# Performance work log

Measured on AMD Instinct MI355X. Metric: run time of the kernel, lower is better.

Reference implementation:

```python
import jax, jax.numpy as jnp
import numpy as np

N_HEADS = 8


def setup_inputs() -> dict:
    key = jax.random.key(0)
    qkv = jax.random.normal(key, (4, 1536, 2048), dtype=jnp.float32)
    return {"qkv": qkv}


def reference(qkv) -> jnp.ndarray:
    bs, width, length = qkv.shape
    assert width % (3 * N_HEADS) == 0
    ch = width // (3 * N_HEADS)
    # [bs*H, 3*ch, T] -> split into q, k, v each [bs*H, ch, T]
    qkv_ = qkv.reshape(bs * N_HEADS, 3 * ch, length)
    q, k, v = qkv_[:, :ch], qkv_[:, ch:2 * ch], qkv_[:, 2 * ch:]
    scale = 1.0 / np.sqrt(np.sqrt(ch)).astype(np.float32)
    # scores [bs*H, T_q, T_k]
    weight = jnp.einsum('bct,bcs->bts', q * scale, k * scale)
    # NOTE: faithful to source — softmax over dim=1 (the query axis t), in float32
    weight = jax.nn.softmax(weight.astype(jnp.float32), axis=1).astype(weight.dtype)
    a = jnp.einsum('bts,bcs->bct', weight, v)  # [bs*H, ch, T]
    return a.reshape(bs, N_HEADS * ch, length)
```

## Files before the change

kernel.cpp:

```cpp
#include <hip/hip_runtime.h>
#include <hip/hip_bf16.h>


#define SEQ   2048
#define CHD   64
#define NHB   32
#define SCALE_QK 0.42466090f

typedef short bf16x8 __attribute__((ext_vector_type(8)));
typedef float f32x4  __attribute__((ext_vector_type(4)));
typedef float f32x16 __attribute__((ext_vector_type(16)));
typedef unsigned int   u32x4 __attribute__((ext_vector_type(4)));
typedef unsigned short us8   __attribute__((ext_vector_type(8)));

extern "C" __device__ float __ocml_native_exp2_f32(float);
#define EXP2(x) __ocml_native_exp2_f32(x)

__device__ __forceinline__ unsigned short f2bf(float f) {
    unsigned int u = __builtin_bit_cast(unsigned int, f);
    u += 0x7FFFu + ((u >> 16) & 1u);
    return (unsigned short)(u >> 16);
}

__device__ __forceinline__ void gl_lds16(const void* g, void* l) {
    __builtin_amdgcn_global_load_lds(
        (const __attribute__((address_space(1))) void*)g,
        (__attribute__((address_space(3))) void*)l, 16, 0, 0);
}

__device__ __forceinline__ unsigned cvtpk(float a, float b) {
    unsigned r;
    asm("v_cvt_pk_bf16_f32 %0, %1, %2" : "=v"(r) : "v"(a), "v"(b));
    return r;
}
__device__ __forceinline__ void plswap(unsigned &a, unsigned &b) {
    asm("v_permlane32_swap_b32 %0, %1" : "+v"(a), "+v"(b));
}

#define ZERO16 {0.f,0.f,0.f,0.f,0.f,0.f,0.f,0.f,0.f,0.f,0.f,0.f,0.f,0.f,0.f,0.f}

__global__ __launch_bounds__(256) void convert_qk(
    const float* __restrict__ qkv, unsigned short* __restrict__ Qt,
    unsigned short* __restrict__ Kt)
{
    __shared__ float Tl[64][129];
    const int bid = blockIdx.x;
    const int head = bid >> 4, t0 = (bid & 15) * 128;
    const int b = head >> 3, h = head & 7;
    const float* base = qkv + (size_t)(b * 1536 + h * 192) * SEQ;
    const int tid = threadIdx.x;
#pragma unroll
    for (int pp = 0; pp < 2; ++pp) {
        const float* src = base + (size_t)(pp ? CHD : 0) * SEQ;
        unsigned short* dst = (pp ? Kt : Qt) + (size_t)head * SEQ * CHD;
        if (pp) __syncthreads();
        for (int e = tid; e < 8192; e += 256) {
            int c = e >> 7, ti = e & 127;
            Tl[c][ti] = src[(size_t)c * SEQ + t0 + ti];
        }
        __syncthreads();
        for (int g = tid; g < 1024; g += 256) {
            int t = g >> 3, cg = g & 7;
            us8 u;
#pragma unroll
            for (int j = 0; j < 8; ++j) u[j] = f2bf(Tl[cg * 8 + j][t] * SCALE_QK);
            *(us8*)(dst + (size_t)(t0 + t) * 64 + ((cg * 8) ^ ((t & 7) << 3))) = u;
        }
    }
}

__global__ __launch_bounds__(512, 2) void stats10_kernel(
    const float* __restrict__ qkv, const unsigned short* __restrict__ Qt,
    const unsigned short* __restrict__ Kt, unsigned short* __restrict__ Vb)
{
    __shared__ __attribute__((aligned(16))) unsigned short Qs[4][4096];
    __shared__ float rlb[256];
    const int bid = blockIdx.x;
    const int bs  = ((bid & 7) << 5) | (bid >> 3);
    const int head = bs >> 3, s0 = (bs & 7) * 256;
    const int b = head >> 3, h = head & 7;
    const char* Qhb = (const char*)(Qt + (size_t)head * SEQ * CHD);
    const unsigned short* Kh = Kt + (size_t)head * SEQ * CHD;
    const int tid = threadIdx.x, w = tid >> 6, l = tid & 63, lo5 = l & 31, hi = l >> 5;
    const int rsw = (lo5 & 7) << 3;

    bf16x8 kfr[4];
#pragma unroll
    for (int kc = 0; kc < 4; ++kc)
        kfr[kc] = *(const bf16x8*)(
            Kh + (size_t)(s0 + w * 32 + lo5) * 64 + (((kc << 4) + (hi << 3)) ^ rsw));

    auto stage = [&](int p, int tc) {
        gl_lds16(Qhb + (size_t)tc * 8192 + tid * 16, &Qs[p][0] + tid * 8);
    };

    float lacc[4] = {0.f, 0.f, 0.f, 0.f};

    stage(0, 0);
    stage(1, 1);
    for (int tc = 0; tc < 32; ++tc) {
        if (tc < 31) asm volatile("s_waitcnt vmcnt(1)" ::: "memory");
        else         asm volatile("s_waitcnt vmcnt(0)" ::: "memory");
        __builtin_amdgcn_s_barrier();
        __builtin_amdgcn_sched_barrier(0);
        if (tc < 30) stage((tc + 2) & 3, tc + 2);
        const unsigned short* qs = &Qs[tc & 3][0];
        __builtin_amdgcn_s_setprio(1);
#pragma unroll
        for (int ts = 0; ts < 2; ++ts) {
            f32x16 s = ZERO16;
#pragma unroll
            for (int kc = 0; kc < 4; ++kc) {
                bf16x8 qa = *(const bf16x8*)(
                    qs + (ts * 32 + lo5) * 64 + (((kc << 4) + (hi << 3)) ^ rsw));
                s = __builtin_amdgcn_mfma_f32_32x32x16_bf16(qa, kfr[kc], s, 0, 0, 0);
            }
#pragma unroll
            for (int r = 0; r < 16; ++r) lacc[r & 3] += EXP2(s[r]);
        }
        __builtin_amdgcn_s_setprio(0);
    }

    float lsum = (lacc[0] + lacc[1]) + (lacc[2] + lacc[3]);
    lsum += __shfl_xor(lsum, 32);
    if (l < 32) rlb[w * 32 + lo5] = 1.0f / lsum;
    __syncthreads();

    const float* vp = qkv + (size_t)(b * 1536 + h * 192 + 2 * CHD) * SEQ;
    unsigned short* Vh = Vb + (size_t)head * SEQ * CHD;
    for (int g = tid; g < 2048; g += 512) {
        int c = g >> 5, si8 = (g & 31) * 8;
        const float* vrow = vp + (size_t)c * SEQ + s0 + si8;
        f32x4 v0 = *(const f32x4*)(vrow);
        f32x4 v1 = *(const f32x4*)(vrow + 4);
        us8 u;
#pragma unroll
        for (int j = 0; j < 4; ++j) u[j]     = f2bf(v0[j] * rlb[si8 + j]);
#pragma unroll
        for (int j = 0; j < 4; ++j) u[4 + j] = f2bf(v1[j] * rlb[si8 + 4 + j]);
        int swb = (si8 & ~63) | ((si8 & 63) ^ ((c & 7) << 3));
        *(us8*)(Vh + (size_t)c * SEQ + s0 + swb) = u;
    }
}

__global__ __launch_bounds__(512, 1) void attn13_kernel(
    const unsigned short* __restrict__ Qt, const unsigned short* __restrict__ Kt,
    const unsigned short* __restrict__ Vb, float* __restrict__ out)
{
    __shared__ __attribute__((aligned(16))) unsigned short KV[4][8192];
    const int bid = blockIdx.x;
    const int bs  = ((bid & 7) << 5) | (bid >> 3);
    const int head = bs >> 3, t0 = (bs & 7) * 256;
    const int b = head >> 3, h = head & 7;
    const int tid = threadIdx.x, w = tid >> 6, l = tid & 63, lo5 = l & 31, hi = l >> 5;
    const int tw = w >> 1, sh = w & 1;
    const int rsw = (lo5 & 7) << 3;
    const unsigned short* Qh = Qt + (size_t)head * SEQ * CHD;
    const char* Khb = (const char*)(Kt + (size_t)head * SEQ * CHD);
    const char* Vhb = (const char*)(Vb + (size_t)head * SEQ * CHD);

    bf16x8 qfA[4], qfB[4];
#pragma unroll
    for (int kc = 0; kc < 4; ++kc) {
        qfA[kc] = *(const bf16x8*)(
            Qh + (size_t)(t0 + tw * 64 + lo5) * 64 + (((kc << 4) + (hi << 3)) ^ rsw));
        qfB[kc] = *(const bf16x8*)(
            Qh + (size_t)(t0 + tw * 64 + 32 + lo5) * 64 + (((kc << 4) + (hi << 3)) ^ rsw));
    }

    f32x16 accA0 = ZERO16, accA1 = ZERO16, accB0 = ZERO16, accB1 = ZERO16;

    const int vc = tid >> 3, vs16 = (tid & 7) * 16;
    auto stage = [&](int p, int cj) {
        unsigned short* kb = &KV[p][0];
        unsigned short* vb = &KV[p][4096];
        gl_lds16(Khb + (size_t)cj * 8192 + tid * 16, kb + tid * 8);
        gl_lds16(Vhb + (size_t)vc * 4096 + (size_t)cj * 128 + vs16, vb + tid * 8);
    };

    stage(0, 0);
    stage(1, 1);

    for (int j = 0; j < 32; ++j) {
        const int p = j & 3;
        if (j < 31) asm volatile("s_waitcnt vmcnt(2)" ::: "memory");
        else        asm volatile("s_waitcnt vmcnt(0)" ::: "memory");
        __builtin_amdgcn_s_barrier();
        __builtin_amdgcn_sched_barrier(0);
        if (j < 30) stage((j + 2) & 3, j + 2);

        const unsigned short* kb = &KV[p][0];
        const unsigned short* vb = &KV[p][4096];

        bf16x8 kf[4], vf0k0, vf0k1, vf1k0, vf1k1;
#pragma unroll
        for (int kc = 0; kc < 4; ++kc)
            kf[kc] = *(const bf16x8*)(
                kb + (sh * 32 + lo5) * 64 + (((kc << 4) + (hi << 3)) ^ rsw));
        vf0k0 = *(const bf16x8*)(vb + (lo5) * 64       + ((sh * 32 +      (hi << 3)) ^ rsw));
        vf0k1 = *(const bf16x8*)(vb + (lo5) * 64       + ((sh * 32 + 16 + (hi << 3)) ^ rsw));
        vf1k0 = *(const bf16x8*)(vb + (32 + lo5) * 64  + ((sh * 32 +      (hi << 3)) ^ rsw));
        vf1k1 = *(const bf16x8*)(vb + (32 + lo5) * 64  + ((sh * 32 + 16 + (hi << 3)) ^ rsw));

        __builtin_amdgcn_s_setprio(1);
        f32x16 SA = ZERO16, SB = ZERO16;
#pragma unroll
        for (int kc = 0; kc < 4; ++kc)
            SA = __builtin_amdgcn_mfma_f32_32x32x16_bf16(kf[kc], qfA[kc], SA, 0, 0, 0);
#pragma unroll
        for (int kc = 0; kc < 4; ++kc)
            SB = __builtin_amdgcn_mfma_f32_32x32x16_bf16(kf[kc], qfB[kc], SB, 0, 0, 0);

        {
            float p16[16];
#pragma unroll
            for (int r = 0; r < 16; ++r) p16[r] = EXP2(SA[r]);
            unsigned w0 = cvtpk(p16[0],  p16[1]),  w1 = cvtpk(p16[2],  p16[3]);
            unsigned w2 = cvtpk(p16[4],  p16[5]),  w3 = cvtpk(p16[6],  p16[7]);
            unsigned w4 = cvtpk(p16[8],  p16[9]),  w5 = cvtpk(p16[10], p16[11]);
            unsigned w6 = cvtpk(p16[12], p16[13]), w7 = cvtpk(p16[14], p16[15]);
            plswap(w0, w2); plswap(w1, w3); plswap(w4, w6); plswap(w5, w7);
            bf16x8 pfA = __builtin_bit_cast(bf16x8, (u32x4){w0, w1, w2, w3});
            bf16x8 pfB = __builtin_bit_cast(bf16x8, (u32x4){w4, w5, w6, w7});
            accA0 = __builtin_amdgcn_mfma_f32_32x32x16_bf16(vf0k0, pfA, accA0, 0, 0, 0);
            accA0 = __builtin_amdgcn_mfma_f32_32x32x16_bf16(vf0k1, pfB, accA0, 0, 0, 0);
            accA1 = __builtin_amdgcn_mfma_f32_32x32x16_bf16(vf1k0, pfA, accA1, 0, 0, 0);
            accA1 = __builtin_amdgcn_mfma_f32_32x32x16_bf16(vf1k1, pfB, accA1, 0, 0, 0);
        }
        {
            float p16[16];
#pragma unroll
            for (int r = 0; r < 16; ++r) p16[r] = EXP2(SB[r]);
            unsigned w0 = cvtpk(p16[0],  p16[1]),  w1 = cvtpk(p16[2],  p16[3]);
            unsigned w2 = cvtpk(p16[4],  p16[5]),  w3 = cvtpk(p16[6],  p16[7]);
            unsigned w4 = cvtpk(p16[8],  p16[9]),  w5 = cvtpk(p16[10], p16[11]);
            unsigned w6 = cvtpk(p16[12], p16[13]), w7 = cvtpk(p16[14], p16[15]);
            plswap(w0, w2); plswap(w1, w3); plswap(w4, w6); plswap(w5, w7);
            bf16x8 pfA = __builtin_bit_cast(bf16x8, (u32x4){w0, w1, w2, w3});
            bf16x8 pfB = __builtin_bit_cast(bf16x8, (u32x4){w4, w5, w6, w7});
            accB0 = __builtin_amdgcn_mfma_f32_32x32x16_bf16(vf0k0, pfA, accB0, 0, 0, 0);
            accB0 = __builtin_amdgcn_mfma_f32_32x32x16_bf16(vf0k1, pfB, accB0, 0, 0, 0);
            accB1 = __builtin_amdgcn_mfma_f32_32x32x16_bf16(vf1k0, pfA, accB1, 0, 0, 0);
            accB1 = __builtin_amdgcn_mfma_f32_32x32x16_bf16(vf1k1, pfB, accB1, 0, 0, 0);
        }
        __builtin_amdgcn_s_setprio(0);
    }

    __syncthreads();
    float* red = (float*)&KV[0][0];
    if (sh == 0) {
        *(f32x16*)(red + (size_t)w * 2048 + l * 16)        = accA1;
        *(f32x16*)(red + (size_t)w * 2048 + 1024 + l * 16) = accB1;
    } else {
        *(f32x16*)(red + (size_t)w * 2048 + l * 16)        = accA0;
        *(f32x16*)(red + (size_t)w * 2048 + 1024 + l * 16) = accB0;
    }
    __syncthreads();
    f32x16 pA = *(const f32x16*)(red + (size_t)(w ^ 1) * 2048 + l * 16);
    f32x16 pB = *(const f32x16*)(red + (size_t)(w ^ 1) * 2048 + 1024 + l * 16);
    f32x16 finA, finB;
    if (sh == 0) { finA = accA0 + pA; finB = accB0 + pB; }
    else         { finA = accA1 + pA; finB = accB1 + pB; }

    float* op = out + (size_t)(b * 512 + h * 64) * SEQ;
    const int tA = t0 + tw * 64 + lo5, tB = tA + 32;
#pragma unroll
    for (int r = 0; r < 16; ++r) {
        int c = sh * 32 + (r & 3) + 8 * (r >> 2) + 4 * hi;
        op[(size_t)c * SEQ + tA] = finA[r];
        op[(size_t)c * SEQ + tB] = finB[r];
    }
}


__device__ __forceinline__ bf16x8 lds_frag(const unsigned short* base, int row, int el) {
    int e = el ^ ((row & 7) << 3);
    return *(const bf16x8*)(base + row * 64 + e);
}

__global__ __launch_bounds__(256) void qkv_stats_kernel(
    const float* __restrict__ qkv, float* __restrict__ m_ws, float* __restrict__ rl_ws)
{
    __shared__ __attribute__((aligned(16))) unsigned short Kl[128 * 64];
    __shared__ __attribute__((aligned(16))) unsigned short Ql[64 * 64];
    const int head = blockIdx.x >> 4, stile = blockIdx.x & 15, s0 = stile * 128;
    const int b = head >> 3, h = head & 7;
    const float* qp = qkv + (size_t)(b * 1536 + h * 192) * SEQ;
    const float* kp = qp + (size_t)CHD * SEQ;
    const int tid = threadIdx.x, w = tid >> 6, l = tid & 63, lg = l >> 4, lr = l & 15;
    for (int idx = tid; idx < 128 * 64; idx += 256) {
        int s = idx & 127, c = idx >> 7;
        Kl[s * 64 + (c ^ ((s & 7) << 3))] = f2bf(kp[(size_t)c * SEQ + s0 + s]);
    }
    float m_run[2] = {-__builtin_inff(), -__builtin_inff()};
    float l_run[2] = {0.f, 0.f};
    for (int chunk = 0; chunk < 32; ++chunk) {
        const int t0 = chunk * 64;
        __syncthreads();
        for (int idx = tid; idx < 64 * 64; idx += 256) {
            int t = idx & 63, c = idx >> 6;
            Ql[t * 64 + (c ^ ((t & 7) << 3))] = f2bf(qp[(size_t)c * SEQ + t0 + t]);
        }
        __syncthreads();
#pragma unroll
        for (int ntl = 0; ntl < 2; ++ntl) {
            const int srow = 16 * (2 * w + ntl) + lr;
            float vals[16];
#pragma unroll
            for (int mt = 0; mt < 4; ++mt) {
                f32x4 sacc = {0.f, 0.f, 0.f, 0.f};
#pragma unroll
                for (int kk = 0; kk < 2; ++kk) {
                    bf16x8 a  = lds_frag(Ql, 16 * mt + lr, 32 * kk + 8 * lg);
                    bf16x8 bk = lds_frag(Kl, srow,         32 * kk + 8 * lg);
                    sacc = __builtin_amdgcn_mfma_f32_16x16x32_bf16(a, bk, sacc, 0, 0, 0);
                }
#pragma unroll
                for (int j = 0; j < 4; ++j) vals[mt * 4 + j] = sacc[j] * 0.125f;
            }
            float cm = vals[0];
#pragma unroll
            for (int i = 1; i < 16; ++i) cm = fmaxf(cm, vals[i]);
            cm = fmaxf(cm, __shfl_xor(cm, 16));
            cm = fmaxf(cm, __shfl_xor(cm, 32));
            float newm = fmaxf(m_run[ntl], cm);
            l_run[ntl] *= __expf(m_run[ntl] - newm);
            m_run[ntl] = newm;
            float ps = 0.f;
#pragma unroll
            for (int i = 0; i < 16; ++i) ps += __expf(vals[i] - newm);
            ps += __shfl_xor(ps, 16);
            ps += __shfl_xor(ps, 32);
            l_run[ntl] += ps;
        }
    }
    if (lg == 0) {
#pragma unroll
        for (int ntl = 0; ntl < 2; ++ntl) {
            int sg = s0 + 16 * (2 * w + ntl) + lr;
            m_ws[head * SEQ + sg]  = m_run[ntl];
            rl_ws[head * SEQ + sg] = 1.0f / l_run[ntl];
        }
    }
}

__global__ __launch_bounds__(256) void qkv_attn_kernel(
    const float* __restrict__ qkv, const float* __restrict__ m_ws,
    const float* __restrict__ rl_ws, float* __restrict__ out)
{
    __shared__ __attribute__((aligned(16))) unsigned short Ql[128 * 64];
    __shared__ __attribute__((aligned(16))) unsigned short Kl[64 * 64];
    __shared__ __attribute__((aligned(16))) unsigned short Vl[64 * 64];
    __shared__ __attribute__((aligned(16))) unsigned short Pl[128 * 64];
    const int head = blockIdx.x >> 4, ttile = blockIdx.x & 15, t0 = ttile * 128;
    const int b = head >> 3, h = head & 7;
    const float* qp  = qkv + (size_t)(b * 1536 + h * 192) * SEQ;
    const float* kp  = qp + (size_t)CHD * SEQ;
    const float* vp  = qp + (size_t)(2 * CHD) * SEQ;
    const float* mh  = m_ws  + head * SEQ;
    const float* rlh = rl_ws + head * SEQ;
    const int tid = threadIdx.x, w = tid >> 6, l = tid & 63, lg = l >> 4, lr = l & 15;
    for (int idx = tid; idx < 128 * 64; idx += 256) {
        int t = idx & 127, c = idx >> 7;
        Ql[t * 64 + (c ^ ((t & 7) << 3))] = f2bf(qp[(size_t)c * SEQ + t0 + t]);
    }
    f32x4 acc[4][2];
#pragma unroll
    for (int i = 0; i < 4; ++i)
#pragma unroll
        for (int j = 0; j < 2; ++j) acc[i][j] = (f32x4){0.f, 0.f, 0.f, 0.f};
    for (int sc = 0; sc < 32; ++sc) {
        const int s0 = sc * 64;
        __syncthreads();
        for (int idx = tid; idx < 64 * 64; idx += 256) {
            int s = idx & 63, c = idx >> 6;
            Kl[s * 64 + (c ^ ((s & 7) << 3))] = f2bf(kp[(size_t)c * SEQ + s0 + s]);
            Vl[c * 64 + (s ^ ((c & 7) << 3))] = f2bf(vp[(size_t)c * SEQ + s0 + s] * rlh[s0 + s]);
        }
        __syncthreads();
        float msv[4];
#pragma unroll
        for (int nts = 0; nts < 4; ++nts) msv[nts] = mh[s0 + 16 * nts + lr];
#pragma unroll
        for (int mts = 0; mts < 2; ++mts) {
            const int trowbase = 16 * (2 * w + mts);
#pragma unroll
            for (int nts = 0; nts < 4; ++nts) {
                f32x4 sa = {0.f, 0.f, 0.f, 0.f};
#pragma unroll
                for (int kk = 0; kk < 2; ++kk) {
                    bf16x8 a  = lds_frag(Ql, trowbase + lr, 32 * kk + 8 * lg);
                    bf16x8 bk = lds_frag(Kl, 16 * nts + lr, 32 * kk + 8 * lg);
                    sa = __builtin_amdgcn_mfma_f32_16x16x32_bf16(a, bk, sa, 0, 0, 0);
                }
                const int scol = 16 * nts + lr;
#pragma unroll
                for (int j = 0; j < 4; ++j) {
                    int trow = trowbase + 4 * lg + j;
                    float p = __expf(sa[j] * 0.125f - msv[nts]);
                    Pl[trow * 64 + (scol ^ ((trow & 7) << 3))] = f2bf(p);
                }
            }
        }
#pragma unroll
        for (int mt = 0; mt < 4; ++mt) {
#pragma unroll
            for (int ntl = 0; ntl < 2; ++ntl) {
                const int trow = 16 * (2 * w + ntl);
#pragma unroll
                for (int kk = 0; kk < 2; ++kk) {
                    bf16x8 a  = lds_frag(Vl, 16 * mt + lr, 32 * kk + 8 * lg);
                    bf16x8 bp = lds_frag(Pl, trow + lr,    32 * kk + 8 * lg);
                    acc[mt][ntl] = __builtin_amdgcn_mfma_f32_16x16x32_bf16(a, bp, acc[mt][ntl], 0, 0, 0);
                }
            }
        }
    }
    float* op = out + (size_t)(b * 512 + h * 64) * SEQ;
#pragma unroll
    for (int mt = 0; mt < 4; ++mt) {
#pragma unroll
        for (int ntl = 0; ntl < 2; ++ntl) {
            int tcol = t0 + 16 * (2 * w + ntl) + lr;
#pragma unroll
            for (int j = 0; j < 4; ++j) {
                int c = 16 * mt + 4 * lg + j;
                op[(size_t)c * SEQ + tcol] = acc[mt][ntl][j];
            }
        }
    }
}

extern "C" void kernel_launch(void* const* d_in, const int* in_sizes, int n_in,
                              void* d_out, int out_size, void* d_ws, size_t ws_size,
                              hipStream_t stream) {
    const float* qkv = (const float*)d_in[0];
    float* out = (float*)d_out;
    (void)in_sizes; (void)n_in; (void)out_size;

    const size_t need = (size_t)3 * NHB * SEQ * CHD * 2;
    if (ws_size >= need) {
        unsigned short* Qt = (unsigned short*)d_ws;
        unsigned short* Kt = Qt + (size_t)NHB * SEQ * CHD;
        unsigned short* Vb = Kt + (size_t)NHB * SEQ * CHD;
        convert_qk    <<<dim3(NHB * 16), dim3(256), 0, stream>>>(qkv, Qt, Kt);
        stats10_kernel<<<dim3(256),      dim3(512), 0, stream>>>(qkv, Qt, Kt, Vb);
        attn13_kernel <<<dim3(256),      dim3(512), 0, stream>>>(Qt, Kt, Vb, out);
    } else {
        float* m_ws  = (float*)d_ws;
        float* rl_ws = m_ws + (size_t)NHB * SEQ;
        qkv_stats_kernel<<<dim3(NHB * 16), dim3(256), 0, stream>>>(qkv, m_ws, rl_ws);
        qkv_attn_kernel <<<dim3(NHB * 16), dim3(256), 0, stream>>>(qkv, m_ws, rl_ws, out);
    }
}
```

Before: 82.80 us.

## Split stats and attention kernels along reduction axis with atomic accumulation

The column-sum stats kernel is split in two. One kernel computes partial sums over half the query range and combines them with atomic adds. A second kernel scales V by the reciprocal sums. The attention kernel likewise splits the key dimension in half across twice as many blocks and accumulates output with atomic adds after memsetting it. This doubles grid size to fill more CUs on a 256-CU part, at the cost of extra memsets, an additional launch, and atomic traffic on the output.

```diff
diff --git a/kernel.cpp b/kernel.cpp
--- a/kernel.cpp
+++ b/kernel.cpp
@@ -69,66 +69,78 @@
     }
 }
 
-__global__ __launch_bounds__(512, 2) void stats10_kernel(
-    const float* __restrict__ qkv, const unsigned short* __restrict__ Qt,
-    const unsigned short* __restrict__ Kt, unsigned short* __restrict__ Vb)
+__global__ __launch_bounds__(512, 4) void statsA_kernel(
+    const unsigned short* __restrict__ Qt, const unsigned short* __restrict__ Kt,
+    float* __restrict__ l_ws)
 {
     __shared__ __attribute__((aligned(16))) unsigned short Qs[4][4096];
+    const int bid = blockIdx.x;
+    const int bs  = ((bid & 7) << 6) | (bid >> 3);
+    const int head = bs >> 4, s0 = ((bs >> 1) & 7) * 256, tH = bs & 1;
+    const char* Qhb = (const char*)(Qt + (size_t)head * SEQ * CHD);
+    const unsigned short* Kh = Kt + (size_t)head * SEQ * CHD;
+    const int tid = threadIdx.x, w = tid >> 6, l = tid & 63, lo5 = l & 31, hi = l >> 5;
+    const int rsw = (lo5 & 7) << 3;
+
+    bf16x8 kfr[4];
+#pragma unroll
+    for (int kc = 0; kc < 4; ++kc)
+        kfr[kc] = *(const bf16x8*)(
+            Kh + (size_t)(s0 + w * 32 + lo5) * 64 + (((kc << 4) + (hi << 3)) ^ rsw));
+
+    auto stage = [&](int p, int tc) {
+        gl_lds16(Qhb + (size_t)(tH * 16 + tc) * 8192 + tid * 16, &Qs[p][0] + tid * 8);
+    };
+
+    float lacc[4] = {0.f, 0.f, 0.f, 0.f};
+
+    stage(0, 0);
+    stage(1, 1);
+    for (int tc = 0; tc < 16; ++tc) {
+        if (tc < 15) asm volatile("s_waitcnt vmcnt(1)" ::: "memory");
+        else         asm volatile("s_waitcnt vmcnt(0)" ::: "memory");
+        __builtin_amdgcn_s_barrier();
+        __builtin_amdgcn_sched_barrier(0);
+        if (tc < 14) stage((tc + 2) & 3, tc + 2);
+        const unsigned short* qs = &Qs[tc & 3][0];
+        __builtin_amdgcn_s_setprio(1);
+#pragma unroll
+        for (int ts = 0; ts < 2; ++ts) {
+            f32x16 s = ZERO16;
+#pragma unroll
+            for (int kc = 0; kc < 4; ++kc) {
+                bf16x8 qa = *(const bf16x8*)(
+                    qs + (ts * 32 + lo5) * 64 + (((kc << 4) + (hi << 3)) ^ rsw));
+                s = __builtin_amdgcn_mfma_f32_32x32x16_bf16(qa, kfr[kc], s, 0, 0, 0);
+            }
+#pragma unroll
+            for (int r = 0; r < 16; ++r) lacc[r & 3] += EXP2(s[r]);
+        }
+        __builtin_amdgcn_s_setprio(0);
+    }
+
+    float lsum = (lacc[0] + lacc[1]) + (lacc[2] + lacc[3]);
+    lsum += __shfl_xor(lsum, 32);
+    if (l < 32) unsafeAtomicAdd(&l_ws[head * SEQ + s0 + w * 32 + lo5], lsum);
+}
+
+__global__ __launch_bounds__(256) void statsB_kernel(
+    const float* __restrict__ qkv, const float* __restrict__ l_ws,
+    unsigned short* __restrict__ Vb)
+{
     __shared__ float rlb[256];
     const int bid = blockIdx.x;
     const int bs  = ((bid & 7) << 5) | (bid >> 3);
     const int head = bs >> 3, s0 = (bs & 7) * 256;
     const int b = head >> 3, h = head & 7;
-    const char* Qhb = (const char*)(Qt + (size_t)head * SEQ * CHD);
-    const unsigned short* Kh = Kt + (size_t)head * SEQ * CHD;
-    const int tid = threadIdx.x, w = tid >> 6, l = tid & 63, lo5 = l & 31, hi = l >> 5;
-    const int rsw = (lo5 & 7) << 3;
-
-    bf16x8 kfr[4];
-#pragma unroll
-    for (int kc = 0; kc < 4; ++kc)
-        kfr[kc] = *(const bf16x8*)(
-            Kh + (size_t)(s0 + w * 32 + lo5) * 64 + (((kc << 4) + (hi << 3)) ^ rsw));
-
-    auto stage = [&](int p, int tc) {
-        gl_lds16(Qhb + (size_t)tc * 8192 + tid * 16, &Qs[p][0] + tid * 8);
-    };
-
-    float lacc[4] = {0.f, 0.f, 0.f, 0.f};
-
-    stage(0, 0);
-    stage(1, 1);
-    for (int tc = 0; tc < 32; ++tc) {
-        if (tc < 31) asm volatile("s_waitcnt vmcnt(1)" ::: "memory");
-        else         asm volatile("s_waitcnt vmcnt(0)" ::: "memory");
-        __builtin_amdgcn_s_barrier();
-        __builtin_amdgcn_sched_barrier(0);
-        if (tc < 30) stage((tc + 2) & 3, tc + 2);
-        const unsigned short* qs = &Qs[tc & 3][0];
-        __builtin_amdgcn_s_setprio(1);
-#pragma unroll
-        for (int ts = 0; ts < 2; ++ts) {
-            f32x16 s = ZERO16;
-#pragma unroll
-            for (int kc = 0; kc < 4; ++kc) {
-                bf16x8 qa = *(const bf16x8*)(
-                    qs + (ts * 32 + lo5) * 64 + (((kc << 4) + (hi << 3)) ^ rsw));
-                s = __builtin_amdgcn_mfma_f32_32x32x16_bf16(qa, kfr[kc], s, 0, 0, 0);
-            }
-#pragma unroll
-            for (int r = 0; r < 16; ++r) lacc[r & 3] += EXP2(s[r]);
-        }
-        __builtin_amdgcn_s_setprio(0);
-    }
-
-    float lsum = (lacc[0] + lacc[1]) + (lacc[2] + lacc[3]);
-    lsum += __shfl_xor(lsum, 32);
-    if (l < 32) rlb[w * 32 + lo5] = 1.0f / lsum;
+    const int tid = threadIdx.x;
+
+    rlb[tid] = 1.0f / l_ws[head * SEQ + s0 + tid];
     __syncthreads();
 
     const float* vp = qkv + (size_t)(b * 1536 + h * 192 + 2 * CHD) * SEQ;
     unsigned short* Vh = Vb + (size_t)head * SEQ * CHD;
-    for (int g = tid; g < 2048; g += 512) {
+    for (int g = tid; g < 2048; g += 256) {
         int c = g >> 5, si8 = (g & 31) * 8;
         const float* vrow = vp + (size_t)c * SEQ + s0 + si8;
         f32x4 v0 = *(const f32x4*)(vrow);
@@ -143,14 +155,15 @@
     }
 }
 
-__global__ __launch_bounds__(512, 1) void attn13_kernel(
+__global__ __launch_bounds__(512, 4) void attnA_kernel(
     const unsigned short* __restrict__ Qt, const unsigned short* __restrict__ Kt,
     const unsigned short* __restrict__ Vb, float* __restrict__ out)
 {
     __shared__ __attribute__((aligned(16))) unsigned short KV[4][8192];
     const int bid = blockIdx.x;
-    const int bs  = ((bid & 7) << 5) | (bid >> 3);
-    const int head = bs >> 3, t0 = (bs & 7) * 256;
+    const int bs  = ((bid & 7) << 6) | (bid >> 3);
+    const int head = bs >> 4, t0 = ((bs >> 1) & 7) * 256, sH = bs & 1;
+    const int cbase = sH * 16;
     const int b = head >> 3, h = head & 7;
     const int tid = threadIdx.x, w = tid >> 6, l = tid & 63, lo5 = l & 31, hi = l >> 5;
     const int tw = w >> 1, sh = w & 1;
@@ -178,16 +191,16 @@
         gl_lds16(Vhb + (size_t)vc * 4096 + (size_t)cj * 128 + vs16, vb + tid * 8);
     };
 
-    stage(0, 0);
-    stage(1, 1);
-
-    for (int j = 0; j < 32; ++j) {
+    stage(0, cbase + 0);
+    stage(1, cbase + 1);
+
+    for (int j = 0; j < 16; ++j) {
         const int p = j & 3;
-        if (j < 31) asm volatile("s_waitcnt vmcnt(2)" ::: "memory");
+        if (j < 15) asm volatile("s_waitcnt vmcnt(2)" ::: "memory");
         else        asm volatile("s_waitcnt vmcnt(0)" ::: "memory");
         __builtin_amdgcn_s_barrier();
         __builtin_amdgcn_sched_barrier(0);
-        if (j < 30) stage((j + 2) & 3, j + 2);
+        if (j < 14) stage((j + 2) & 3, cbase + j + 2);
 
         const unsigned short* kb = &KV[p][0];
         const unsigned short* vb = &KV[p][4096];
@@ -267,8 +280,8 @@
 #pragma unroll
     for (int r = 0; r < 16; ++r) {
         int c = sh * 32 + (r & 3) + 8 * (r >> 2) + 4 * hi;
-        op[(size_t)c * SEQ + tA] = finA[r];
-        op[(size_t)c * SEQ + tB] = finB[r];
+        unsafeAtomicAdd(&op[(size_t)c * SEQ + tA], finA[r]);
+        unsafeAtomicAdd(&op[(size_t)c * SEQ + tB], finB[r]);
     }
 }
 
@@ -436,16 +449,21 @@
                               hipStream_t stream) {
     const float* qkv = (const float*)d_in[0];
     float* out = (float*)d_out;
-    (void)in_sizes; (void)n_in; (void)out_size;
-
-    const size_t need = (size_t)3 * NHB * SEQ * CHD * 2;
+    (void)in_sizes; (void)n_in;
+
+    const size_t bufE = (size_t)NHB * SEQ * CHD;
+    const size_t need = 3 * bufE * 2 + (size_t)NHB * SEQ * 4;
     if (ws_size >= need) {
         unsigned short* Qt = (unsigned short*)d_ws;
-        unsigned short* Kt = Qt + (size_t)NHB * SEQ * CHD;
-        unsigned short* Vb = Kt + (size_t)NHB * SEQ * CHD;
-        convert_qk    <<<dim3(NHB * 16), dim3(256), 0, stream>>>(qkv, Qt, Kt);
-        stats10_kernel<<<dim3(256),      dim3(512), 0, stream>>>(qkv, Qt, Kt, Vb);
-        attn13_kernel <<<dim3(256),      dim3(512), 0, stream>>>(Qt, Kt, Vb, out);
+        unsigned short* Kt = Qt + bufE;
+        unsigned short* Vb = Kt + bufE;
+        float* l_ws = (float*)(Vb + bufE);
+        hipMemsetAsync(l_ws, 0, (size_t)NHB * SEQ * 4, stream);
+        hipMemsetAsync(out, 0, (size_t)out_size * 4, stream);
+        convert_qk   <<<dim3(NHB * 16), dim3(256), 0, stream>>>(qkv, Qt, Kt);
+        statsA_kernel<<<dim3(512),      dim3(512), 0, stream>>>(Qt, Kt, l_ws);
+        statsB_kernel<<<dim3(256),      dim3(256), 0, stream>>>(qkv, l_ws, Vb);
+        attnA_kernel <<<dim3(512),      dim3(512), 0, stream>>>(Qt, Kt, Vb, out);
     } else {
         float* m_ws  = (float*)d_ws;
         float* rl_ws = m_ws + (size_t)NHB * SEQ;
```

Result: slower. 249.1 us (+200.8%).
